# Performance work log

Hardware: AMD Instinct MI355X
Metric: run time of the kernel (lower is better)

Reference implementation:

```python
import jax, jax.numpy as jnp
import numpy as np

# Orbital structure for basis {A: [2s, 2p, 1d]} -> full_basis l values
LS = [0, 0, 1, 1, 2]
DIMS = [2 * l + 1 for l in LS]            # [1,1,3,3,5]
OFFS = np.concatenate([[0], np.cumsum(DIMS)]).astype(int)
NORB = int(sum(DIMS))                      # 13

# Upper-triangular orbital-pair layout of the flat feature vector
PAIRS = []
_off = 0
for _i in range(len(LS)):
    for _j in range(_i, len(LS)):
        PAIRS.append((_i, _j, _off))
        _off += DIMS[_i] * DIMS[_j]
FEAT_DIM = _off                            # 107

N_ATOMS, N_EDGES, N_KPTS = 256, 4096, 4


def _assemble_blocks(feat):
    """[B, FEAT_DIM] -> [B, NORB, NORB], upper-tri orbital blocks, 0.5 on diagonal pairs."""
    B = feat.shape[0]
    blk = jnp.zeros((B, NORB, NORB), feat.dtype)
    for (i, j, o) in PAIRS:
        di, dj = DIMS[i], DIMS[j]
        f = 0.5 if i == j else 1.0
        blk = blk.at[:, OFFS[i]:OFFS[i] + di, OFFS[j]:OFFS[j] + dj].set(
            f * feat[:, o:o + di * dj].reshape(B, di, dj))
    return blk


def setup_inputs() -> dict:
    key = jax.random.key(0)
    k1, k2, k3, k4, k5 = jax.random.split(key, 5)
    return {
        "orbpair_hopping": jax.random.normal(k1, (N_EDGES, FEAT_DIM), jnp.float32),
        "orbpair_onsite": jax.random.normal(k2, (N_ATOMS, FEAT_DIM), jnp.float32),
        "kpoints": jax.random.uniform(k3, (N_KPTS, 3), jnp.float32),
        "edge_cell_shift": jax.random.randint(k4, (N_EDGES, 3), -3, 4).astype(jnp.float32),
        "edge_index": jax.random.randint(k5, (2, N_EDGES), 0, N_ATOMS),
    }


def reference(orbpair_hopping, orbpair_onsite, kpoints, edge_cell_shift, edge_index):
    hop = _assemble_blocks(orbpair_hopping)      # [E, norb, norb]
    onsite = _assemble_blocks(orbpair_onsite)    # [N, norb, norb]
    N, K = onsite.shape[0], kpoints.shape[0]
    cplx = jnp.complex64

    # phase[k, e] = exp(-i 2pi k . R_e)
    phase = jnp.exp(-2j * jnp.pi * (kpoints @ edge_cell_shift.T)).astype(cplx)  # [K, E]

    # H(k) in block form [K, N, N, norb, norb]
    blk = jnp.zeros((K, N, N, NORB, NORB), cplx)
    ar = jnp.arange(N)
    blk = blk.at[:, ar, ar].set(onsite.astype(cplx)[None])  # diagonal onsite blocks
    ei, ej = edge_index[0], edge_index[1]
    blk = blk.at[:, ei, ej].add(phase[:, :, None, None] * hop.astype(cplx)[None])

    H = blk.transpose(0, 1, 3, 2, 4).reshape(K, N * NORB, N * NORB)
    return H + jnp.conj(jnp.swapaxes(H, 1, 2))  # hermitianize
```

## Files before the change

### kernel.cpp

```cpp
#include <hip/hip_runtime.h>

#define NORB 13
#define FEAT 107
#define TWO_PI 6.28318530717958647692f
#define NN 3328
#define ROWF (NN * 2)
#define R4 (NN / 2)
#define EMAX 4096
#define CAP 128
#define MAXS 48

__device__ int   g_acnt[256];
__device__ int   g_items[256 * CAP];
__device__ int   g_ovh[256];
__device__ int   g_ovnxt[2 * EMAX];
__device__ int   g_ovitem[2 * EMAX];
__device__ float g_phases[EMAX * 8];

__device__ __forceinline__ void map_pq(int p, int q, int& idx, float& scl) {
    const int DIMS[5] = {1, 1, 3, 3, 5};
    const int OFFS[5] = {0, 1, 2, 5, 8};
    idx = -1; scl = 0.0f;
    int o = 0;
    #pragma unroll
    for (int i = 0; i < 5; ++i) {
        #pragma unroll
        for (int j = i; j < 5; ++j) {
            int di = DIMS[i], dj = DIMS[j];
            if (p >= OFFS[i] && p < OFFS[i] + di && q >= OFFS[j] && q < OFFS[j] + dj) {
                idx = o + (p - OFFS[i]) * dj + (q - OFFS[j]);
                scl = (i == j) ? 0.5f : 1.0f;
            }
            o += di * dj;
        }
    }
}


__global__ void init_kernel() {
    int t = threadIdx.x;
    g_acnt[t] = 0;
    g_ovh[t] = -1;
}

__global__ void fill_kernel(const int* __restrict__ eidx, const float* __restrict__ kpt,
                            const float* __restrict__ shf, int E, int K) {
    int tid = blockIdx.x * blockDim.x + threadIdx.x;
    if (tid >= 2 * E) return;
    int e = tid >> 1, dir = tid & 1;
    int ei = eidx[e], ej = eidx[E + e];
    int a = dir ? ej : ei;
    int b = dir ? ei : ej;
    int pk = (b << 13) | (e << 1) | dir;
    int slot = atomicAdd(&g_acnt[a], 1);
    if (slot < CAP) {
        g_items[a * CAP + slot] = pk;
    } else {
        int old = atomicExch(&g_ovh[a], tid);
        g_ovnxt[tid] = old;
        g_ovitem[tid] = pk;
    }
    if (dir == 0) {
        float rx = shf[e * 3 + 0], ry = shf[e * 3 + 1], rz = shf[e * 3 + 2];
        for (int k = 0; k < K; ++k) {
            float th = -TWO_PI * (kpt[k * 3] * rx + kpt[k * 3 + 1] * ry + kpt[k * 3 + 2] * rz);
            float s, c;
            __sincosf(th, &s, &c);
            g_phases[e * 8 + k * 2]     = c;
            g_phases[e * 8 + k * 2 + 1] = s;
        }
    }
}

__global__ __launch_bounds__(256)
void fused3_kernel(const float* __restrict__ hop, const float* __restrict__ ons,
                   float* __restrict__ out) {
    int z = blockIdx.x;
    int k = z >> 9;
    int a = (z >> 1) & 255;
    int half = z & 1;
    int rbase = half ? 7 : 0;
    int nrows = half ? 6 : 7;
    int t = threadIdx.x;

    __shared__ int ilist[CAP];
    __shared__ unsigned char present[256];
    __shared__ unsigned char smap[256];
    __shared__ unsigned char sblk[MAXS];
    __shared__ unsigned long long wmask[4];
    __shared__ float2 pblk[MAXS][91];

    int n = g_acnt[a];
    present[t] = 0;
    __syncthreads();
    int nb = n < CAP ? n : CAP;
    for (int i = t; i < nb; i += 256) {
        int pk = g_items[a * CAP + i];
        ilist[i] = pk;
        present[(pk >> 13) & 255] = 1;
    }
    if (t == 0) present[a] = 1;
    __syncthreads();

    unsigned long long m = __ballot(present[t] != 0);
    int w = t >> 6;
    if ((t & 63) == 0) wmask[w] = m;
    __syncthreads();
    int nslots = __popcll(wmask[0]) + __popcll(wmask[1]) +
                 __popcll(wmask[2]) + __popcll(wmask[3]);
    bool fallback = (n > CAP) || (nslots > MAXS);

    if (!fallback) {
        if (present[t]) {
            int pre = 0;
            #pragma unroll
            for (int i = 0; i < 4; ++i) if (i < w) pre += __popcll(wmask[i]);
            pre += __popcll(wmask[w] & ((1ull << (t & 63)) - 1ull));
            smap[t] = (unsigned char)pre;
            sblk[pre] = (unsigned char)t;
        } else {
            smap[t] = 255;
        }
        __syncthreads();

        float2* pf = &pblk[0][0];
        for (int i = t; i < nslots * 91; i += 256) pf[i] = make_float2(0.f, 0.f);
        __syncthreads();

        if (t < 91) {
            int p = rbase + t / 13, q = t % 13;
            int i0, i1; float s0, s1;
            map_pq(p, q, i0, s0);
            map_pq(q, p, i1, s1);
            {
                const float* f = ons + (long)a * FEAT;
                float v = 0.f;
                if (i0 >= 0) v += s0 * f[i0];
                if (i1 >= 0) v += s1 * f[i1];
                pblk[smap[a]][t].x += v;
            }
            for (int i = 0; i < nb; ++i) {
                int pk = ilist[i];
                int b = (pk >> 13) & 255;
                int e = (pk >> 1) & 4095;
                int dir = pk & 1;
                int s = smap[b];
                float hv = dir ? ((i1 >= 0) ? s1 * hop[(long)e * FEAT + i1] : 0.f)
                               : ((i0 >= 0) ? s0 * hop[(long)e * FEAT + i0] : 0.f);
                float pr = g_phases[e * 8 + k * 2];
                float pi = g_phases[e * 8 + k * 2 + 1];
                float2 v = pblk[s][t];
                v.x += pr * hv;
                v.y += (dir ? -pi : pi) * hv;
                pblk[s][t] = v;
            }
        }
        __syncthreads();

        float4* out4 = (float4*)out;
        int ntask8 = nslots * nrows * 8;
        for (int it0 = t; it0 < ntask8; it0 += 256) {
            int lane = it0 & 7;
            int task = it0 >> 3;
            int s = task % nslots;
            int rr = task / nslots;
            int b = sblk[s];
            int fb = (13 * b) >> 1;
            int fe = (13 * b + 12) >> 1;
            int f = fb + lane;
            if (f > fe) continue;
            int c0 = 2 * f, c1 = c0 + 1;
            float4 v;
            {
                int bc = (unsigned)c0 / 13u;
                int mm = smap[bc];
                if (mm != 255) { float2 pv = pblk[mm][rr * 13 + (c0 - 13 * bc)]; v.x = pv.x; v.y = pv.y; }
                else           { v.x = 0.f; v.y = 0.f; }
            }
            {
                int bc = (unsigned)c1 / 13u;
                int mm = smap[bc];
                if (mm != 255) { float2 pv = pblk[mm][rr * 13 + (c1 - 13 * bc)]; v.z = pv.x; v.w = pv.y; }
                else           { v.z = 0.f; v.w = 0.f; }
            }
            long off4 = (long)(k * NN + a * 13 + rbase + rr) * R4 + f;
            out4[off4] = v;
        }

        float4 z4 = make_float4(0.f, 0.f, 0.f, 0.f);
        float4* out4c = (float4*)out;
        for (int rr = 0; rr < nrows; ++rr) {
            long rowb = (long)(k * NN + a * 13 + rbase + rr) * R4;
            for (int f = t; f < R4; f += 256) {
                int b0 = (unsigned)(2 * f) / 13u;
                int b1 = (unsigned)(2 * f + 1) / 13u;
                if (smap[b0] != 255 || smap[b1] != 255) continue;
                out4c[rowb + f] = z4;
            }
        }
    } else {
        float4 z4 = make_float4(0.f, 0.f, 0.f, 0.f);
        float4* out4 = (float4*)out;
        for (int rr = 0; rr < nrows; ++rr) {
            long rowb = (long)(k * NN + a * 13 + rbase + rr) * R4;
            for (int f = t; f < R4; f += 256)
                out4[rowb + f] = z4;
        }
        __syncthreads();
        int maxt = nrows * 13;
        if (t < maxt) {
            int p = rbase + t / 13, q = t % 13;
            int i0, i1; float s0, s1;
            map_pq(p, q, i0, s0);
            map_pq(q, p, i1, s1);
            {
                const float* f = ons + (long)a * FEAT;
                float v = 0.f;
                if (i0 >= 0) v += s0 * f[i0];
                if (i1 >= 0) v += s1 * f[i1];
                long off = (long)(k * NN + a * 13 + p) * ROWF + (a * 13 + q) * 2;
                atomicAdd(&out[off], v);
            }
            int nbl = n < CAP ? n : CAP;
            for (int i = 0; i < nbl; ++i) {
                int pk = g_items[a * CAP + i];
                int b = (pk >> 13) & 255, e = (pk >> 1) & 4095, dir = pk & 1;
                float hv = dir ? ((i1 >= 0) ? s1 * hop[(long)e * FEAT + i1] : 0.f)
                               : ((i0 >= 0) ? s0 * hop[(long)e * FEAT + i0] : 0.f);
                float pr = g_phases[e * 8 + k * 2];
                float pi = g_phases[e * 8 + k * 2 + 1];
                long off = (long)(k * NN + a * 13 + p) * ROWF + (b * 13 + q) * 2;
                atomicAdd(&out[off], pr * hv);
                atomicAdd(&out[off + 1], (dir ? -pi : pi) * hv);
            }
            for (int it = g_ovh[a]; it >= 0; it = g_ovnxt[it]) {
                int pk = g_ovitem[it];
                int b = (pk >> 13) & 255, e = (pk >> 1) & 4095, dir = pk & 1;
                float hv = dir ? ((i1 >= 0) ? s1 * hop[(long)e * FEAT + i1] : 0.f)
                               : ((i0 >= 0) ? s0 * hop[(long)e * FEAT + i0] : 0.f);
                float pr = g_phases[e * 8 + k * 2];
                float pi = g_phases[e * 8 + k * 2 + 1];
                long off = (long)(k * NN + a * 13 + p) * ROWF + (b * 13 + q) * 2;
                atomicAdd(&out[off], pr * hv);
                atomicAdd(&out[off + 1], (dir ? -pi : pi) * hv);
            }
        }
    }
}


__global__ void zero_kernel(float4* __restrict__ out, long n4) {
    long i = (long)blockIdx.x * blockDim.x + threadIdx.x;
    long stride = (long)gridDim.x * blockDim.x;
    float4 zz = make_float4(0.f, 0.f, 0.f, 0.f);
    for (; i < n4; i += stride) out[i] = zz;
}

template <int CPX>
__global__ void onsite_kernel(const float* __restrict__ onsite, float* __restrict__ out,
                              int K, long nn) {
    int a = blockIdx.x;
    int t = threadIdx.x;
    if (t >= NORB * NORB) return;
    int p = t / NORB, q = t % NORB;
    int i1, i2; float s1, s2;
    map_pq(p, q, i1, s1);
    map_pq(q, p, i2, s2);
    const float* f = onsite + (long)a * FEAT;
    float v = 0.0f;
    if (i1 >= 0) v += s1 * f[i1];
    if (i2 >= 0) v += s2 * f[i2];
    long row = (long)a * NORB + p;
    long col = (long)a * NORB + q;
    for (int k = 0; k < K; ++k) {
        long off = (((long)k * nn + row) * nn + col) * CPX;
        out[off] = v;
    }
}

template <int CPX>
__global__ void edge_kernel(const float* __restrict__ hop, const float* __restrict__ kpts,
                            const float* __restrict__ shift, const int* __restrict__ eidx,
                            float* __restrict__ out, int E, int K, long nn) {
    int e = blockIdx.x;
    int t = threadIdx.x;
    __shared__ float phc[16], phs[16];
    int ei = eidx[e];
    int ej = eidx[E + e];
    if (t < K && t < 16) {
        float rx = shift[(long)e * 3 + 0];
        float ry = shift[(long)e * 3 + 1];
        float rz = shift[(long)e * 3 + 2];
        float th = -TWO_PI * (kpts[t * 3 + 0] * rx + kpts[t * 3 + 1] * ry + kpts[t * 3 + 2] * rz);
        float s, c;
        __sincosf(th, &s, &c);
        phc[t] = c; phs[t] = s;
    }
    __syncthreads();
    if (t >= NORB * NORB) return;
    int p = t / NORB, q = t % NORB;
    int idx; float scl;
    map_pq(p, q, idx, scl);
    if (idx < 0) return;
    float v = scl * hop[(long)e * FEAT + idx];
    long r1 = (long)ei * NORB + p, c1 = (long)ej * NORB + q;
    long r2 = (long)ej * NORB + q, c2 = (long)ei * NORB + p;
    for (int k = 0; k < K; ++k) {
        float pr = phc[k], pi = phs[k];
        long o1 = (((long)k * nn + r1) * nn + c1) * CPX;
        long o2 = (((long)k * nn + r2) * nn + c2) * CPX;
        atomicAdd(&out[o1], pr * v);
        atomicAdd(&out[o2], pr * v);
        if (CPX == 2) {
            atomicAdd(&out[o1 + 1], pi * v);
            atomicAdd(&out[o2 + 1], -pi * v);
        }
    }
}


extern "C" void kernel_launch(void* const* d_in, const int* in_sizes, int n_in,
                              void* d_out, int out_size, void* d_ws, size_t ws_size,
                              hipStream_t stream) {
    const float* hop  = (const float*)d_in[0];
    const float* ons  = (const float*)d_in[1];
    const float* kpt  = (const float*)d_in[2];
    const float* shf  = (const float*)d_in[3];
    const int*   eidx = (const int*)d_in[4];

    int E = in_sizes[0] / FEAT;
    int N = in_sizes[1] / FEAT;
    int K = in_sizes[2] / 3;
    long nn = (long)N * NORB;

    float* out = (float*)d_out;
    long knn2 = (long)K * nn * nn * 2;

    bool fast = (N == 256) && (K == 4) && (E <= EMAX) &&
                ((long)out_size == knn2);

    if (fast) {
        init_kernel<<<1, 256, 0, stream>>>();
        fill_kernel<<<(2 * E + 255) / 256, 256, 0, stream>>>(eidx, kpt, shf, E, K);
        fused3_kernel<<<2048, 256, 0, stream>>>(hop, ons, out);
    } else {
        int cpx = ((long)out_size >= knn2) ? 2 : 1;
        long n4 = (long)out_size / 4;
        zero_kernel<<<2048, 256, 0, stream>>>((float4*)out, n4);
        if (cpx == 2) {
            onsite_kernel<2><<<N, 192, 0, stream>>>(ons, out, K, nn);
            edge_kernel<2><<<E, 192, 0, stream>>>(hop, kpt, shf, eidx, out, E, K, nn);
        } else {
            onsite_kernel<1><<<N, 192, 0, stream>>>(ons, out, K, nn);
            edge_kernel<1><<<E, 192, 0, stream>>>(hop, kpt, shf, eidx, out, E, K, nn);
        }
    }
}
```

Before: 79.58 us.

## Fuse edge bucketing and phase computation into single monolithic row kernel

Removes the init and fill kernels. Each block now scans the whole edge list itself to collect its atom's incident edges into shared memory, and computes the per-edge phases locally. The output write is also merged into one pass per row that writes either block values or zeros, replacing the separate nonzero and zero-fill passes. This saves two kernel launches and the global scratch traffic, at the cost of every one of the 2048 blocks redundantly reading all edge indices.

```diff
diff --git a/kernel.cpp b/kernel.cpp
--- a/kernel.cpp
+++ b/kernel.cpp
@@ -9,13 +9,6 @@
 #define EMAX 4096
 #define CAP 128
 #define MAXS 48
-
-__device__ int   g_acnt[256];
-__device__ int   g_items[256 * CAP];
-__device__ int   g_ovh[256];
-__device__ int   g_ovnxt[2 * EMAX];
-__device__ int   g_ovitem[2 * EMAX];
-__device__ float g_phases[EMAX * 8];
 
 __device__ __forceinline__ void map_pq(int p, int q, int& idx, float& scl) {
     const int DIMS[5] = {1, 1, 3, 3, 5};
@@ -36,45 +29,10 @@
     }
 }
 
-
-__global__ void init_kernel() {
-    int t = threadIdx.x;
-    g_acnt[t] = 0;
-    g_ovh[t] = -1;
-}
-
-__global__ void fill_kernel(const int* __restrict__ eidx, const float* __restrict__ kpt,
-                            const float* __restrict__ shf, int E, int K) {
-    int tid = blockIdx.x * blockDim.x + threadIdx.x;
-    if (tid >= 2 * E) return;
-    int e = tid >> 1, dir = tid & 1;
-    int ei = eidx[e], ej = eidx[E + e];
-    int a = dir ? ej : ei;
-    int b = dir ? ei : ej;
-    int pk = (b << 13) | (e << 1) | dir;
-    int slot = atomicAdd(&g_acnt[a], 1);
-    if (slot < CAP) {
-        g_items[a * CAP + slot] = pk;
-    } else {
-        int old = atomicExch(&g_ovh[a], tid);
-        g_ovnxt[tid] = old;
-        g_ovitem[tid] = pk;
-    }
-    if (dir == 0) {
-        float rx = shf[e * 3 + 0], ry = shf[e * 3 + 1], rz = shf[e * 3 + 2];
-        for (int k = 0; k < K; ++k) {
-            float th = -TWO_PI * (kpt[k * 3] * rx + kpt[k * 3 + 1] * ry + kpt[k * 3 + 2] * rz);
-            float s, c;
-            __sincosf(th, &s, &c);
-            g_phases[e * 8 + k * 2]     = c;
-            g_phases[e * 8 + k * 2 + 1] = s;
-        }
-    }
-}
-
 __global__ __launch_bounds__(256)
-void fused3_kernel(const float* __restrict__ hop, const float* __restrict__ ons,
-                   float* __restrict__ out) {
+void mono_kernel(const float* __restrict__ hop, const float* __restrict__ ons,
+                 const float* __restrict__ kpt, const float* __restrict__ shf,
+                 const int* __restrict__ eidx, float* __restrict__ out, int E) {
     int z = blockIdx.x;
     int k = z >> 9;
     int a = (z >> 1) & 255;
@@ -84,23 +42,38 @@
     int t = threadIdx.x;
 
     __shared__ int ilist[CAP];
+    __shared__ int nmatch;
+    __shared__ float2 phl[CAP];
     __shared__ unsigned char present[256];
     __shared__ unsigned char smap[256];
-    __shared__ unsigned char sblk[MAXS];
     __shared__ unsigned long long wmask[4];
     __shared__ float2 pblk[MAXS][91];
 
-    int n = g_acnt[a];
+    if (t == 0) nmatch = 0;
     present[t] = 0;
     __syncthreads();
+
+    for (int e = t; e < E; e += 256) {
+        int ei = eidx[e], ej = eidx[E + e];
+        if (ei == a) { int s = atomicAdd(&nmatch, 1); if (s < CAP) ilist[s] = (ej << 13) | (e << 1); }
+        if (ej == a) { int s = atomicAdd(&nmatch, 1); if (s < CAP) ilist[s] = (ei << 13) | (e << 1) | 1; }
+    }
+    __syncthreads();
+    int n = nmatch;
     int nb = n < CAP ? n : CAP;
+
+    for (int i = t; i < nb; i += 256) present[ilist[i] >> 13] = 1;
+    if (t == 0) present[a] = 1;
+    __syncthreads();
+
+    float kx = kpt[k * 3], ky = kpt[k * 3 + 1], kz = kpt[k * 3 + 2];
     for (int i = t; i < nb; i += 256) {
-        int pk = g_items[a * CAP + i];
-        ilist[i] = pk;
-        present[(pk >> 13) & 255] = 1;
-    }
-    if (t == 0) present[a] = 1;
-    __syncthreads();
+        int e = (ilist[i] >> 1) & 4095;
+        float th = -TWO_PI * (kx * shf[e * 3] + ky * shf[e * 3 + 1] + kz * shf[e * 3 + 2]);
+        float s, c;
+        __sincosf(th, &s, &c);
+        phl[i] = make_float2(c, s);
+    }
 
     unsigned long long m = __ballot(present[t] != 0);
     int w = t >> 6;
@@ -108,16 +81,16 @@
     __syncthreads();
     int nslots = __popcll(wmask[0]) + __popcll(wmask[1]) +
                  __popcll(wmask[2]) + __popcll(wmask[3]);
-    bool fallback = (n > CAP) || (nslots > MAXS);
-
-    if (!fallback) {
+
+    int nloc = nrows * 13;
+
+    if (n <= CAP && nslots <= MAXS) {
         if (present[t]) {
             int pre = 0;
             #pragma unroll
             for (int i = 0; i < 4; ++i) if (i < w) pre += __popcll(wmask[i]);
             pre += __popcll(wmask[w] & ((1ull << (t & 63)) - 1ull));
             smap[t] = (unsigned char)pre;
-            sblk[pre] = (unsigned char)t;
         } else {
             smap[t] = 255;
         }
@@ -127,7 +100,7 @@
         for (int i = t; i < nslots * 91; i += 256) pf[i] = make_float2(0.f, 0.f);
         __syncthreads();
 
-        if (t < 91) {
+        if (t < nloc) {
             int p = rbase + t / 13, q = t % 13;
             int i0, i1; float s0, s1;
             map_pq(p, q, i0, s0);
@@ -141,61 +114,33 @@
             }
             for (int i = 0; i < nb; ++i) {
                 int pk = ilist[i];
-                int b = (pk >> 13) & 255;
+                int b = pk >> 13;
                 int e = (pk >> 1) & 4095;
                 int dir = pk & 1;
-                int s = smap[b];
                 float hv = dir ? ((i1 >= 0) ? s1 * hop[(long)e * FEAT + i1] : 0.f)
                                : ((i0 >= 0) ? s0 * hop[(long)e * FEAT + i0] : 0.f);
-                float pr = g_phases[e * 8 + k * 2];
-                float pi = g_phases[e * 8 + k * 2 + 1];
-                float2 v = pblk[s][t];
-                v.x += pr * hv;
-                v.y += (dir ? -pi : pi) * hv;
-                pblk[s][t] = v;
+                float2 ph = phl[i];
+                float2 v = pblk[smap[b]][t];
+                v.x += ph.x * hv;
+                v.y += (dir ? -ph.y : ph.y) * hv;
+                pblk[smap[b]][t] = v;
             }
         }
         __syncthreads();
 
         float4* out4 = (float4*)out;
-        int ntask8 = nslots * nrows * 8;
-        for (int it0 = t; it0 < ntask8; it0 += 256) {
-            int lane = it0 & 7;
-            int task = it0 >> 3;
-            int s = task % nslots;
-            int rr = task / nslots;
-            int b = sblk[s];
-            int fb = (13 * b) >> 1;
-            int fe = (13 * b + 12) >> 1;
-            int f = fb + lane;
-            if (f > fe) continue;
-            int c0 = 2 * f, c1 = c0 + 1;
-            float4 v;
-            {
-                int bc = (unsigned)c0 / 13u;
-                int mm = smap[bc];
-                if (mm != 255) { float2 pv = pblk[mm][rr * 13 + (c0 - 13 * bc)]; v.x = pv.x; v.y = pv.y; }
-                else           { v.x = 0.f; v.y = 0.f; }
-            }
-            {
-                int bc = (unsigned)c1 / 13u;
-                int mm = smap[bc];
-                if (mm != 255) { float2 pv = pblk[mm][rr * 13 + (c1 - 13 * bc)]; v.z = pv.x; v.w = pv.y; }
-                else           { v.z = 0.f; v.w = 0.f; }
-            }
-            long off4 = (long)(k * NN + a * 13 + rbase + rr) * R4 + f;
-            out4[off4] = v;
-        }
-
-        float4 z4 = make_float4(0.f, 0.f, 0.f, 0.f);
-        float4* out4c = (float4*)out;
         for (int rr = 0; rr < nrows; ++rr) {
             long rowb = (long)(k * NN + a * 13 + rbase + rr) * R4;
+            int rloc = rr * 13;
             for (int f = t; f < R4; f += 256) {
-                int b0 = (unsigned)(2 * f) / 13u;
-                int b1 = (unsigned)(2 * f + 1) / 13u;
-                if (smap[b0] != 255 || smap[b1] != 255) continue;
-                out4c[rowb + f] = z4;
+                int c0 = 2 * f, c1 = c0 + 1;
+                int b0 = (unsigned)c0 / 13u;
+                int b1 = (unsigned)c1 / 13u;
+                int m0 = smap[b0], m1 = smap[b1];
+                float4 v = make_float4(0.f, 0.f, 0.f, 0.f);
+                if (m0 != 255) { float2 pv = pblk[m0][rloc + (c0 - 13 * b0)]; v.x = pv.x; v.y = pv.y; }
+                if (m1 != 255) { float2 pv = pblk[m1][rloc + (c1 - 13 * b1)]; v.z = pv.x; v.w = pv.y; }
+                out4[rowb + f] = v;
             }
         }
     } else {
@@ -203,12 +148,10 @@
         float4* out4 = (float4*)out;
         for (int rr = 0; rr < nrows; ++rr) {
             long rowb = (long)(k * NN + a * 13 + rbase + rr) * R4;
-            for (int f = t; f < R4; f += 256)
-                out4[rowb + f] = z4;
+            for (int f = t; f < R4; f += 256) out4[rowb + f] = z4;
         }
         __syncthreads();
-        int maxt = nrows * 13;
-        if (t < maxt) {
+        if (t < nloc) {
             int p = rbase + t / 13, q = t % 13;
             int i0, i1; float s0, s1;
             map_pq(p, q, i0, s0);
@@ -221,28 +164,34 @@
                 long off = (long)(k * NN + a * 13 + p) * ROWF + (a * 13 + q) * 2;
                 atomicAdd(&out[off], v);
             }
-            int nbl = n < CAP ? n : CAP;
-            for (int i = 0; i < nbl; ++i) {
-                int pk = g_items[a * CAP + i];
-                int b = (pk >> 13) & 255, e = (pk >> 1) & 4095, dir = pk & 1;
-                float hv = dir ? ((i1 >= 0) ? s1 * hop[(long)e * FEAT + i1] : 0.f)
-                               : ((i0 >= 0) ? s0 * hop[(long)e * FEAT + i0] : 0.f);
-                float pr = g_phases[e * 8 + k * 2];
-                float pi = g_phases[e * 8 + k * 2 + 1];
-                long off = (long)(k * NN + a * 13 + p) * ROWF + (b * 13 + q) * 2;
-                atomicAdd(&out[off], pr * hv);
-                atomicAdd(&out[off + 1], (dir ? -pi : pi) * hv);
-            }
-            for (int it = g_ovh[a]; it >= 0; it = g_ovnxt[it]) {
-                int pk = g_ovitem[it];
-                int b = (pk >> 13) & 255, e = (pk >> 1) & 4095, dir = pk & 1;
-                float hv = dir ? ((i1 >= 0) ? s1 * hop[(long)e * FEAT + i1] : 0.f)
-                               : ((i0 >= 0) ? s0 * hop[(long)e * FEAT + i0] : 0.f);
-                float pr = g_phases[e * 8 + k * 2];
-                float pi = g_phases[e * 8 + k * 2 + 1];
-                long off = (long)(k * NN + a * 13 + p) * ROWF + (b * 13 + q) * 2;
-                atomicAdd(&out[off], pr * hv);
-                atomicAdd(&out[off + 1], (dir ? -pi : pi) * hv);
+            if (n <= CAP) {
+                for (int i = 0; i < nb; ++i) {
+                    int pk = ilist[i];
+                    int b = pk >> 13, e = (pk >> 1) & 4095, dir = pk & 1;
+                    float hv = dir ? ((i1 >= 0) ? s1 * hop[(long)e * FEAT + i1] : 0.f)
+                                   : ((i0 >= 0) ? s0 * hop[(long)e * FEAT + i0] : 0.f);
+                    float2 ph = phl[i];
+                    long off = (long)(k * NN + a * 13 + p) * ROWF + (b * 13 + q) * 2;
+                    atomicAdd(&out[off], ph.x * hv);
+                    atomicAdd(&out[off + 1], (dir ? -ph.y : ph.y) * hv);
+                }
+            } else {
+                for (int e = 0; e < E; ++e) {
+                    int ei = eidx[e], ej = eidx[E + e];
+                    #pragma unroll
+                    for (int dir = 0; dir < 2; ++dir) {
+                        int sa = dir ? ej : ei, b = dir ? ei : ej;
+                        if (sa != a) continue;
+                        float hv = dir ? ((i1 >= 0) ? s1 * hop[(long)e * FEAT + i1] : 0.f)
+                                       : ((i0 >= 0) ? s0 * hop[(long)e * FEAT + i0] : 0.f);
+                        float th = -TWO_PI * (kx * shf[e*3] + ky * shf[e*3+1] + kz * shf[e*3+2]);
+                        float s, c;
+                        __sincosf(th, &s, &c);
+                        long off = (long)(k * NN + a * 13 + p) * ROWF + (b * 13 + q) * 2;
+                        atomicAdd(&out[off], c * hv);
+                        atomicAdd(&out[off + 1], (dir ? -s : s) * hv);
+                    }
+                }
             }
         }
     }
@@ -340,9 +289,7 @@
                 ((long)out_size == knn2);
 
     if (fast) {
-        init_kernel<<<1, 256, 0, stream>>>();
-        fill_kernel<<<(2 * E + 255) / 256, 256, 0, stream>>>(eidx, kpt, shf, E, K);
-        fused3_kernel<<<2048, 256, 0, stream>>>(hop, ons, out);
+        mono_kernel<<<2048, 256, 0, stream>>>(hop, ons, kpt, shf, eidx, out, E);
     } else {
         int cpx = ((long)out_size >= knn2) ? 2 : 1;
         long n4 = (long)out_size / 4;
```

Result: no change. 79.68 us (+0.1%).
